# Kernel optimization log

Measured on AMD Instinct MI355X. Metric: run time of the kernel, lower is better.

## Reference

```python
import jax, jax.numpy as jnp
import numpy as np

ALPHA = 0.01
GAMMA = 4.0
SPATIAL_WEIGHT = 0.3
SEQ_LEN = 1024
LINE_WINDOW = 2


def setup_inputs() -> dict:
    key = jax.random.key(0)
    k1, k2, k3 = jax.random.split(key, 3)
    B, S, C = 64, SEQ_LEN, 8
    pred = jax.random.normal(k1, (B * S, C), dtype=jnp.float32)
    target = (jax.random.uniform(k2, (B * S, C)) < 0.05).astype(jnp.float32)
    # line indices: monotone non-decreasing within each sequence, ~256 lines
    lines = jnp.sort(
        jax.random.randint(k3, (B, S), 0, 256, dtype=jnp.int32), axis=-1
    ).reshape(-1)
    return {"pred": pred, "target": target, "token_to_line": lines}


def _spatial_penalty(pred, target, token_to_line):
    # pred/target: [B*S, C], token_to_line: [B*S]
    C = pred.shape[1]
    B = pred.shape[0] // SEQ_LEN if pred.shape[0] > SEQ_LEN else 1
    p = pred.reshape(B, SEQ_LEN, C)
    t = target.reshape(B, SEQ_LEN, C)
    l = token_to_line.reshape(B, SEQ_LEN)

    # nearby_mask[b,i,j] = |line_j - line_i| <= 2 and j != i
    diff = jnp.abs(l[:, :, None] - l[:, None, :])          # [B,S,S]
    mask = (diff <= LINE_WINDOW) & ~jnp.eye(SEQ_LEN, dtype=bool)[None]
    maskf = mask.astype(p.dtype)

    counts = maskf.sum(-1)                                  # [B,S]
    # sum of all nearby target entries (summed over classes), per token
    nearby_tgt_sum = jnp.einsum('bij,bj->bi', maskf, t.sum(-1))  # [B,S]
    # mean of sigmoid(pred) over nearby tokens
    sig = jax.nn.sigmoid(p)                                 # [B,S,C]
    sig_mean = jnp.einsum('bij,bjc->bic', maskf, sig) / jnp.maximum(counts, 1.0)[..., None]

    cond = (counts > 0) & (nearby_tgt_sum > 0)              # [B,S]
    penalty = jnp.where(cond[..., None], sig_mean * 0.1, 0.0)
    return penalty.reshape(-1, C)


def reference(pred, target, token_to_line):
    # numerically stable BCE-with-logits (reduction='none')
    bce = jnp.maximum(pred, 0.0) - pred * target + jnp.log1p(jnp.exp(-jnp.abs(pred)))
    pt = jnp.exp(-bce)
    focal = ALPHA * (1.0 - pt) ** GAMMA * bce
    focal = focal + SPATIAL_WEIGHT * _spatial_penalty(pred, target, token_to_line)
    return focal.mean()  # reduction='mean'
```

## Files before the change

### kernel.cpp

```cpp
#include <hip/hip_runtime.h>
#include <math.h>

#define SEQ_LEN 1024
#define NCLASS 8
#define NLINES 256
#define ALPHA_C 0.01f
#define SPW 0.3f
#define MAGIC 0x5EED5EEDu
#define BLOCK 512
#define TOK_PER_THREAD (SEQ_LEN / BLOCK)

__global__ __launch_bounds__(BLOCK) void fused_kernel(
    const float* __restrict__ pred,
    const float* __restrict__ target,
    const int* __restrict__ lines,
    unsigned long long* __restrict__ slots,
    float* __restrict__ out,
    float inv_total, int nblocks)
{
    __shared__ float binCnt[NLINES];
    __shared__ float binT[NLINES];
    __shared__ float binS[NLINES];
    __shared__ float wCnt[NLINES];
    __shared__ float wT[NLINES];
    __shared__ float wS[NLINES];
    __shared__ float wavesum[BLOCK / 64];

    const int b = blockIdx.x;
    const int tid = threadIdx.x;
    const int lane = tid & 63;

    if (tid < NLINES) {
        binCnt[tid] = 0.f;
        binT[tid] = 0.f;
        binS[tid] = 0.f;
    }
    __syncthreads();

    float sg[TOK_PER_THREAD][NCLASS];
    float tsumk[TOK_PER_THREAD];
    float sgsumk[TOK_PER_THREAD];
    int lk[TOK_PER_THREAD];
    unsigned tmask[TOK_PER_THREAD];

    #pragma unroll
    for (int k = 0; k < TOK_PER_THREAD; ++k) {
        const int token = b * SEQ_LEN + k * BLOCK + tid;
        const int l = lines[token];
        lk[k] = l;
        const float4 p0 = ((const float4*)pred)[token * 2];
        const float4 p1 = ((const float4*)pred)[token * 2 + 1];
        const float4 t0 = ((const float4*)target)[token * 2];
        const float4 t1 = ((const float4*)target)[token * 2 + 1];
        const float px[NCLASS] = {p0.x, p0.y, p0.z, p0.w, p1.x, p1.y, p1.z, p1.w};

        const float ts = t0.x + t0.y + t0.z + t0.w + t1.x + t1.y + t1.z + t1.w;
        tsumk[k] = ts;
        unsigned m = 0;
        m |= (t0.x > 0.5f) ? 1u : 0u;
        m |= (t0.y > 0.5f) ? 2u : 0u;
        m |= (t0.z > 0.5f) ? 4u : 0u;
        m |= (t0.w > 0.5f) ? 8u : 0u;
        m |= (t1.x > 0.5f) ? 16u : 0u;
        m |= (t1.y > 0.5f) ? 32u : 0u;
        m |= (t1.z > 0.5f) ? 64u : 0u;
        m |= (t1.w > 0.5f) ? 128u : 0u;
        tmask[k] = m;

        float ssum = 0.f;
        #pragma unroll
        for (int c = 0; c < NCLASS; ++c) {
            const float e = __expf(-px[c]);
            const float s = 1.f / (1.f + e);
            sg[k][c] = s;
            ssum += s;
        }
        sgsumk[k] = ssum;

        float rc = 1.f, rt = ts, rs = ssum;
        #pragma unroll
        for (int off = 1; off < 64; off <<= 1) {
            const int   ln = __shfl_down(l,  off, 64);
            const float ac = __shfl_down(rc, off, 64);
            const float at = __shfl_down(rt, off, 64);
            const float as = __shfl_down(rs, off, 64);
            const bool same = (lane + off < 64) && (ln == l);
            if (same) { rc += ac; rt += at; rs += as; }
        }
        const int lprev = __shfl_up(l, 1, 64);
        const bool head = (lane == 0) || (lprev != l);
        if (head) {
            atomicAdd(&binCnt[l], rc);
            atomicAdd(&binT[l], rt);
            atomicAdd(&binS[l], rs);
        }
    }
    __syncthreads();

    if (tid < NLINES) {
        const int lo = (tid - 2 < 0) ? 0 : tid - 2;
        const int hi = (tid + 2 > NLINES - 1) ? NLINES - 1 : tid + 2;
        float cs = 0.f, ts2 = 0.f, ss = 0.f;
        for (int v = lo; v <= hi; ++v) {
            cs += binCnt[v];
            ts2 += binT[v];
            ss += binS[v];
        }
        wCnt[tid] = cs;
        wT[tid] = ts2;
        wS[tid] = ss;
    }
    __syncthreads();

    float lsum = 0.f;
    #pragma unroll
    for (int k = 0; k < TOK_PER_THREAD; ++k) {
        const int l = lk[k];
        const float counts = wCnt[l] - 1.f;
        const float ntgt = wT[l] - tsumk[k];
        const bool cond = (counts > 0.f) && (ntgt > 0.f);
        const float pfac = cond ? (SPW * 0.1f / counts) : 0.f;

        float fsum = 0.f;
        #pragma unroll
        for (int c = 0; c < NCLASS; ++c) {
            const float s = sg[k][c];
            const bool pos = (tmask[k] >> c) & 1u;
            const float pt = pos ? s : 1.f - s;
            const float om = 1.f - pt;
            const float bce = -__logf(pt);
            const float om2 = om * om;
            fsum += om2 * om2 * bce;
        }
        lsum += ALPHA_C * fsum + pfac * (wS[l] - sgsumk[k]);
    }

    #pragma unroll
    for (int off = 32; off > 0; off >>= 1)
        lsum += __shfl_xor(lsum, off, 64);
    if (lane == 0) wavesum[tid >> 6] = lsum;
    __syncthreads();

    if (tid == 0) {
        float partial = 0.f;
        #pragma unroll
        for (int w = 0; w < BLOCK / 64; ++w) partial += wavesum[w];
        partial *= inv_total;
        const unsigned long long payload =
            ((unsigned long long)MAGIC << 32) | (unsigned long long)__float_as_uint(partial);
        __hip_atomic_store(&slots[b], payload, __ATOMIC_RELEASE,
                           __HIP_MEMORY_SCOPE_AGENT);
    }
    __syncthreads();

    if (b == 0 && tid < 64) {
        float v = 0.f;
        if (tid < nblocks) {
            unsigned long long s;
            do {
                s = __hip_atomic_load(&slots[tid], __ATOMIC_ACQUIRE,
                                      __HIP_MEMORY_SCOPE_AGENT);
            } while ((unsigned)(s >> 32) != MAGIC);
            v = __uint_as_float((unsigned)s);
        }
        #pragma unroll
        for (int off = 32; off > 0; off >>= 1)
            v += __shfl_xor(v, off, 64);
        if (tid == 0) out[0] = v;
    }
}

extern "C" void kernel_launch(void* const* d_in, const int* in_sizes, int n_in,
                              void* d_out, int out_size, void* d_ws, size_t ws_size,
                              hipStream_t stream) {
    const float* pred   = (const float*)d_in[0];
    const float* target = (const float*)d_in[1];
    const int*   lines  = (const int*)d_in[2];
    float* out = (float*)d_out;
    unsigned long long* slots = (unsigned long long*)d_ws;

    const int n_tokens = in_sizes[2];
    const int B = n_tokens / SEQ_LEN;
    const float inv_total = 1.0f / (float)in_sizes[0];

    fused_kernel<<<B, BLOCK, 0, stream>>>(pred, target, lines, slots, out,
                                          inv_total, B);
}
```

Baseline: 61.88 us.

## Use one token per thread and pack count with target sum in one float

The block grows from 512 to 1024 threads, so each thread handles one token instead of two, which drops the per-thread arrays and the token loop. The per-line count and target sum are packed into one float (count times 4096 plus tsum), cutting the shuffles and shared-memory atomics in the segmented reduction. They are unpacked with floorf after the window sum. This relies on tsum per window staying below 4096 and the packed value staying exact in float. With 1024 threads per block and 64 blocks, occupancy per CU and register pressure change as well.

```diff
diff --git a/kernel.cpp b/kernel.cpp
--- a/kernel.cpp
+++ b/kernel.cpp
@@ -7,8 +7,8 @@
 #define ALPHA_C 0.01f
 #define SPW 0.3f
 #define MAGIC 0x5EED5EEDu
-#define BLOCK 512
-#define TOK_PER_THREAD (SEQ_LEN / BLOCK)
+#define BLOCK 1024
+#define PACK 4096.0f
 
 __global__ __launch_bounds__(BLOCK) void fused_kernel(
     const float* __restrict__ pred,
@@ -18,8 +18,7 @@
     float* __restrict__ out,
     float inv_total, int nblocks)
 {
-    __shared__ float binCnt[NLINES];
-    __shared__ float binT[NLINES];
+    __shared__ float binCT[NLINES];
     __shared__ float binS[NLINES];
     __shared__ float wCnt[NLINES];
     __shared__ float wT[NLINES];
@@ -31,67 +30,54 @@
     const int lane = tid & 63;
 
     if (tid < NLINES) {
-        binCnt[tid] = 0.f;
-        binT[tid] = 0.f;
+        binCT[tid] = 0.f;
         binS[tid] = 0.f;
     }
     __syncthreads();
 
-    float sg[TOK_PER_THREAD][NCLASS];
-    float tsumk[TOK_PER_THREAD];
-    float sgsumk[TOK_PER_THREAD];
-    int lk[TOK_PER_THREAD];
-    unsigned tmask[TOK_PER_THREAD];
+    const int token = b * SEQ_LEN + tid;
+    const int l = lines[token];
+    const float4 p0 = ((const float4*)pred)[token * 2];
+    const float4 p1 = ((const float4*)pred)[token * 2 + 1];
+    const float4 t0 = ((const float4*)target)[token * 2];
+    const float4 t1 = ((const float4*)target)[token * 2 + 1];
+    const float px[NCLASS] = {p0.x, p0.y, p0.z, p0.w, p1.x, p1.y, p1.z, p1.w};
 
+    const float tsum = t0.x + t0.y + t0.z + t0.w + t1.x + t1.y + t1.z + t1.w;
+    unsigned tmask = 0;
+    tmask |= (t0.x > 0.5f) ? 1u : 0u;
+    tmask |= (t0.y > 0.5f) ? 2u : 0u;
+    tmask |= (t0.z > 0.5f) ? 4u : 0u;
+    tmask |= (t0.w > 0.5f) ? 8u : 0u;
+    tmask |= (t1.x > 0.5f) ? 16u : 0u;
+    tmask |= (t1.y > 0.5f) ? 32u : 0u;
+    tmask |= (t1.z > 0.5f) ? 64u : 0u;
+    tmask |= (t1.w > 0.5f) ? 128u : 0u;
+
+    float sg[NCLASS];
+    float sgsum = 0.f;
     #pragma unroll
-    for (int k = 0; k < TOK_PER_THREAD; ++k) {
-        const int token = b * SEQ_LEN + k * BLOCK + tid;
-        const int l = lines[token];
-        lk[k] = l;
-        const float4 p0 = ((const float4*)pred)[token * 2];
-        const float4 p1 = ((const float4*)pred)[token * 2 + 1];
-        const float4 t0 = ((const float4*)target)[token * 2];
-        const float4 t1 = ((const float4*)target)[token * 2 + 1];
-        const float px[NCLASS] = {p0.x, p0.y, p0.z, p0.w, p1.x, p1.y, p1.z, p1.w};
+    for (int c = 0; c < NCLASS; ++c) {
+        const float e = __expf(-px[c]);
+        const float s = 1.f / (1.f + e);
+        sg[c] = s;
+        sgsum += s;
+    }
 
-        const float ts = t0.x + t0.y + t0.z + t0.w + t1.x + t1.y + t1.z + t1.w;
-        tsumk[k] = ts;
-        unsigned m = 0;
-        m |= (t0.x > 0.5f) ? 1u : 0u;
-        m |= (t0.y > 0.5f) ? 2u : 0u;
-        m |= (t0.z > 0.5f) ? 4u : 0u;
-        m |= (t0.w > 0.5f) ? 8u : 0u;
-        m |= (t1.x > 0.5f) ? 16u : 0u;
-        m |= (t1.y > 0.5f) ? 32u : 0u;
-        m |= (t1.z > 0.5f) ? 64u : 0u;
-        m |= (t1.w > 0.5f) ? 128u : 0u;
-        tmask[k] = m;
-
-        float ssum = 0.f;
-        #pragma unroll
-        for (int c = 0; c < NCLASS; ++c) {
-            const float e = __expf(-px[c]);
-            const float s = 1.f / (1.f + e);
-            sg[k][c] = s;
-            ssum += s;
-        }
-        sgsumk[k] = ssum;
-
-        float rc = 1.f, rt = ts, rs = ssum;
+    {
+        float rp = PACK + tsum;
+        float rs = sgsum;
         #pragma unroll
         for (int off = 1; off < 64; off <<= 1) {
             const int   ln = __shfl_down(l,  off, 64);
-            const float ac = __shfl_down(rc, off, 64);
-            const float at = __shfl_down(rt, off, 64);
+            const float ap = __shfl_down(rp, off, 64);
             const float as = __shfl_down(rs, off, 64);
             const bool same = (lane + off < 64) && (ln == l);
-            if (same) { rc += ac; rt += at; rs += as; }
+            if (same) { rp += ap; rs += as; }
         }
         const int lprev = __shfl_up(l, 1, 64);
-        const bool head = (lane == 0) || (lprev != l);
-        if (head) {
-            atomicAdd(&binCnt[l], rc);
-            atomicAdd(&binT[l], rt);
+        if ((lane == 0) || (lprev != l)) {
+            atomicAdd(&binCT[l], rp);
             atomicAdd(&binS[l], rs);
         }
     }
@@ -100,39 +86,37 @@
     if (tid < NLINES) {
         const int lo = (tid - 2 < 0) ? 0 : tid - 2;
         const int hi = (tid + 2 > NLINES - 1) ? NLINES - 1 : tid + 2;
-        float cs = 0.f, ts2 = 0.f, ss = 0.f;
+        float cp = 0.f, ss = 0.f;
         for (int v = lo; v <= hi; ++v) {
-            cs += binCnt[v];
-            ts2 += binT[v];
+            cp += binCT[v];
             ss += binS[v];
         }
-        wCnt[tid] = cs;
-        wT[tid] = ts2;
+        const float cnt = floorf(cp / PACK);
+        wCnt[tid] = cnt;
+        wT[tid] = cp - cnt * PACK;
         wS[tid] = ss;
     }
     __syncthreads();
 
-    float lsum = 0.f;
-    #pragma unroll
-    for (int k = 0; k < TOK_PER_THREAD; ++k) {
-        const int l = lk[k];
+    float lsum;
+    {
         const float counts = wCnt[l] - 1.f;
-        const float ntgt = wT[l] - tsumk[k];
+        const float ntgt = wT[l] - tsum;
         const bool cond = (counts > 0.f) && (ntgt > 0.f);
         const float pfac = cond ? (SPW * 0.1f / counts) : 0.f;
 
         float fsum = 0.f;
         #pragma unroll
         for (int c = 0; c < NCLASS; ++c) {
-            const float s = sg[k][c];
-            const bool pos = (tmask[k] >> c) & 1u;
+            const float s = sg[c];
+            const bool pos = (tmask >> c) & 1u;
             const float pt = pos ? s : 1.f - s;
             const float om = 1.f - pt;
             const float bce = -__logf(pt);
             const float om2 = om * om;
             fsum += om2 * om2 * bce;
         }
-        lsum += ALPHA_C * fsum + pfac * (wS[l] - sgsumk[k]);
+        lsum = ALPHA_C * fsum + pfac * (wS[l] - sgsum);
     }
 
     #pragma unroll
```

New measurement: 61.83 us. About the same (-0.1%).
